# Performance work log

Measured on AMD Instinct MI355X. Metric: run time of the kernel, lower is better.

## Reference

```python
import jax, jax.numpy as jnp
import numpy as np

HEADS = 8
EPS = 1e-5

def setup_inputs() -> dict:
    key = jax.random.key(0)
    ks = jax.random.split(key, 4)
    B, S, N, C = 1, 256, 384, 512
    msa = jax.random.normal(ks[0], (B, S, N, C), dtype=jnp.float32)
    mask = jnp.ones((B, S), dtype=jnp.int32)
    Wqkv = jax.random.normal(ks[1], (3 * C, C), dtype=jnp.float32) * (C ** -0.5)
    bqkv = jnp.zeros((3 * C,), dtype=jnp.float32)
    Wout = jax.random.normal(ks[2], (C, C), dtype=jnp.float32) * (C ** -0.5)
    bout = jnp.zeros((C,), dtype=jnp.float32)
    gamma = jnp.ones((C,), dtype=jnp.float32)
    beta = jnp.zeros((C,), dtype=jnp.float32)
    return {"msa": msa, "mask": mask, "Wqkv": Wqkv, "bqkv": bqkv,
            "Wout": Wout, "bout": bout, "gamma": gamma, "beta": beta}

def reference(msa, mask, Wqkv, bqkv, Wout, bout, gamma, beta):
    B, S, N, C = msa.shape
    H = HEADS
    Dh = C // H
    scale = Dh ** -0.5
    msa_t = jnp.transpose(msa, (0, 2, 1, 3))            # [B,N,S,C]
    qkv = msa_t @ Wqkv.T + bqkv                          # [B,N,S,3C]
    qkv = qkv.reshape(B, N, S, 3, H, Dh)
    q, k, v = qkv[..., 0, :, :], qkv[..., 1, :, :], qkv[..., 2, :, :]  # [B,N,S,H,Dh]
    attn = jnp.einsum('bnshc,bnthc->bhst', q, k) * scale  # reduce over N and head-dim
    attn = jnp.where(mask[:, None, None, :] == 0, -1e9, attn)
    attn = jax.nn.softmax(attn, axis=-1)                 # [B,H,S,S]
    out = jnp.einsum('bhst,bnthc->bnshc', attn, v).reshape(B, N, S, C)
    out = jnp.transpose(out, (0, 2, 1, 3))               # [B,S,N,C]
    out = out @ Wout.T + bout
    x = msa + out
    mu = jnp.mean(x, axis=-1, keepdims=True)
    var = jnp.mean((x - mu) ** 2, axis=-1, keepdims=True)
    return (x - mu) * jax.lax.rsqrt(var + EPS) * gamma + beta
```

## Files before the change

kernel.cpp:

```cpp
#include <hip/hip_runtime.h>

#define S_ 256
#define N_ 384
#define C_ 512
#define H_ 8
#define R_ (N_*S_)
#define SPLITK 16
#define NPK (N_/SPLITK)

typedef _Float16 f16;
typedef _Float16 f16x8 __attribute__((ext_vector_type(8)));
typedef _Float16 f16x4 __attribute__((ext_vector_type(4)));
typedef float f32x4 __attribute__((ext_vector_type(4)));

#define MFMA16(a,b,c) __builtin_amdgcn_mfma_f32_16x16x32_f16(a,b,c,0,0,0)

typedef __attribute__((address_space(3))) unsigned int as3_u32;
typedef __attribute__((address_space(1))) const unsigned int as1_u32;

__device__ __forceinline__ void gl_lds16(const void* g, void* l) {
    __builtin_amdgcn_global_load_lds((as1_u32*)(unsigned long long)g,
                                     (as3_u32*)(unsigned long long)l, 16, 0, 0);
}

__device__ __forceinline__ int swz_off(int row, int g) {
    return row*64 + (((g) ^ (row & 7)) << 3);
}

__global__ __launch_bounds__(256) void k_prep(const float* __restrict__ Wqkv,
                                              const float* __restrict__ Wout,
                                              f16* __restrict__ Wq16, f16* __restrict__ Wo16) {
    int i = blockIdx.x * 256 + threadIdx.x;
    if (i < 1536 * C_) Wq16[i] = (f16)Wqkv[i];
    if (i < C_ * C_)   Wo16[i] = (f16)Wout[i];
}

__global__ __launch_bounds__(256) void k_cast(const float* __restrict__ msa,
                                              f16* __restrict__ msaT) {
    int t = blockIdx.x * 256 + threadIdx.x;
    int r = t >> 6, cg = t & 63;
    int n = r >> 8, s = r & 255;
    const float* src = msa + (s * N_ + n) * C_ + (cg << 3);
    float4 lo = *(const float4*)src;
    float4 hi = *(const float4*)(src + 4);
    f16x8 v;
    v[0]=(f16)lo.x; v[1]=(f16)lo.y; v[2]=(f16)lo.z; v[3]=(f16)lo.w;
    v[4]=(f16)hi.x; v[5]=(f16)hi.y; v[6]=(f16)hi.z; v[7]=(f16)hi.w;
    *(f16x8*)(msaT + r * C_ + (cg << 3)) = v;
}

__global__ __launch_bounds__(256) void k_qkv(const f16* __restrict__ msaT,
                                             const f16* __restrict__ W,
                                             const float* __restrict__ bqkv,
                                             f16* __restrict__ qk,
                                             f16* __restrict__ vT) {
    int wg = (blockIdx.x & 7) * 1152 + (blockIdx.x >> 3);
    int bx = wg / 12, by = wg % 12;
    int j0 = by << 7;
    int tid = threadIdx.x, lane = tid & 63, wid = tid >> 6;
    int wr = (wid >> 1) << 6, wc = (wid & 1) << 6;
    __shared__ f16 As[128 * 64];
    __shared__ f16 Bs[128 * 64];
    const f16* Abase = msaT + (bx << 7) * C_;
    const f16* Bbase = W + j0 * C_;
    f32x4 acc[4][4] = {};
    for (int kt = 0; kt < 8; ++kt) {
        int c0 = kt << 6;
        __syncthreads();
#pragma unroll
        for (int i = 0; i < 4; ++i) {
            int id = (i << 8) + tid;
            int row = id >> 3, g = (id & 7) ^ (row & 7);
            int lofs = ((i << 8) + (wid << 6)) << 4;
            gl_lds16(Abase + row * C_ + c0 + (g << 3), (char*)As + lofs);
            gl_lds16(Bbase + row * C_ + c0 + (g << 3), (char*)Bs + lofs);
        }
        __syncthreads();
#pragma unroll
        for (int ks = 0; ks < 64; ks += 32) {
            int kg = (ks >> 3) + (lane >> 4);
            f16x8 af[4], bf[4];
#pragma unroll
            for (int m = 0; m < 4; ++m)
                af[m] = *(const f16x8*)&As[swz_off(wr + (m << 4) + (lane & 15), kg)];
#pragma unroll
            for (int j = 0; j < 4; ++j)
                bf[j] = *(const f16x8*)&Bs[swz_off(wc + (j << 4) + (lane & 15), kg)];
#pragma unroll
            for (int m = 0; m < 4; ++m)
#pragma unroll
                for (int j = 0; j < 4; ++j)
                    acc[m][j] = MFMA16(af[m], bf[j], acc[m][j]);
        }
    }
#pragma unroll
    for (int m = 0; m < 4; ++m) {
        int rloc = wr + (m << 4) + ((lane >> 4) << 2);
        int r0 = (bx << 7) + rloc;
        if (by < 8) {
#pragma unroll
            for (int j = 0; j < 4; ++j) {
                int jc = j0 + wc + (j << 4) + (lane & 15);
                float bv = bqkv[jc];
#pragma unroll
                for (int q = 0; q < 4; ++q)
                    qk[(r0 + q) * 1024 + jc] = (f16)(acc[m][j][q] + bv);
            }
        } else {
            int n = bx >> 1, sBase = ((bx & 1) << 7) + rloc;
#pragma unroll
            for (int j = 0; j < 4; ++j) {
                int jl = (j0 - 1024) + wc + (j << 4) + (lane & 15);
                float bv = bqkv[1024 + jl];
                f16x4 vv;
#pragma unroll
                for (int q = 0; q < 4; ++q) vv[q] = (f16)(acc[m][j][q] + bv);
                *(f16x4*)(vT + ((n * H_ + (jl >> 6)) * 64 + (jl & 63)) * S_ + sBase) = vv;
            }
        }
    }
}

__global__ __launch_bounds__(256) void k_logits(const f16* __restrict__ qk,
                                                float* __restrict__ logP) {
    int wg = (blockIdx.x & 7) * 64 + (blockIdx.x >> 3);
    int sk = wg >> 5, rem = wg & 31, h = rem >> 2, sb = (rem >> 1) & 1, tb = rem & 1;
    int s0 = sb << 7, t0 = tb << 7, n0 = sk * NPK;
    int tid = threadIdx.x, lane = tid & 63, wid = tid >> 6;
    int wr = (wid >> 1) << 6, wc = (wid & 1) << 6;
    __shared__ f16 As[128 * 64];
    __shared__ f16 Bs[128 * 64];
    f32x4 acc[4][4] = {};
    for (int ni = 0; ni < NPK; ++ni) {
        int n = n0 + ni;
        const f16* Abase = qk + (n * S_ + s0) * 1024 + (h << 6);
        const f16* Bbase = qk + (n * S_ + t0) * 1024 + 512 + (h << 6);
        __syncthreads();
#pragma unroll
        for (int i = 0; i < 4; ++i) {
            int id = (i << 8) + tid;
            int row = id >> 3, g = (id & 7) ^ (row & 7);
            int lofs = ((i << 8) + (wid << 6)) << 4;
            gl_lds16(Abase + row * 1024 + (g << 3), (char*)As + lofs);
            gl_lds16(Bbase + row * 1024 + (g << 3), (char*)Bs + lofs);
        }
        __syncthreads();
#pragma unroll
        for (int ks = 0; ks < 64; ks += 32) {
            int kg = (ks >> 3) + (lane >> 4);
            f16x8 af[4], bf[4];
#pragma unroll
            for (int m = 0; m < 4; ++m)
                af[m] = *(const f16x8*)&As[swz_off(wr + (m << 4) + (lane & 15), kg)];
#pragma unroll
            for (int j = 0; j < 4; ++j)
                bf[j] = *(const f16x8*)&Bs[swz_off(wc + (j << 4) + (lane & 15), kg)];
#pragma unroll
            for (int m = 0; m < 4; ++m)
#pragma unroll
                for (int j = 0; j < 4; ++j)
                    acc[m][j] = MFMA16(af[m], bf[j], acc[m][j]);
        }
    }
#pragma unroll
    for (int m = 0; m < 4; ++m) {
        int rloc = wr + (m << 4) + ((lane >> 4) << 2);
#pragma unroll
        for (int j = 0; j < 4; ++j) {
            int tc = t0 + wc + (j << 4) + (lane & 15);
#pragma unroll
            for (int q = 0; q < 4; ++q)
                logP[((sk * H_ + h) * S_ + s0 + rloc + q) * S_ + tc] = acc[m][j][q];
        }
    }
}

__global__ __launch_bounds__(256) void k_softmax(const float* __restrict__ logP,
                                                 const int* __restrict__ mask,
                                                 f16* __restrict__ attn) {
    int hs = blockIdx.x;
    int t = threadIdx.x, lane = t & 63, wid = t >> 6;
    float v = 0.f;
#pragma unroll
    for (int sk = 0; sk < SPLITK; ++sk)
        v += logP[(sk * H_ * S_ + hs) * S_ + t];
    v *= 0.125f;
    if (mask[t] == 0) v = -1e9f;
    __shared__ float redm[4], reds[4];
    float m_ = v;
    for (int o = 32; o > 0; o >>= 1) m_ = fmaxf(m_, __shfl_xor(m_, o));
    if (lane == 0) redm[wid] = m_;
    __syncthreads();
    float bm = fmaxf(fmaxf(redm[0], redm[1]), fmaxf(redm[2], redm[3]));
    float e = __expf(v - bm);
    float s_ = e;
    for (int o = 32; o > 0; o >>= 1) s_ += __shfl_xor(s_, o);
    if (lane == 0) reds[wid] = s_;
    __syncthreads();
    float tot = reds[0] + reds[1] + reds[2] + reds[3];
    attn[hs * S_ + t] = (f16)(e / tot);
}

__global__ __launch_bounds__(256) void k_pv(const f16* __restrict__ attn,
                                            const f16* __restrict__ vT,
                                            f16* __restrict__ attn_out) {
    int n = blockIdx.x >> 3, h = blockIdx.x & 7;
    int tid = threadIdx.x, lane = tid & 63, wid = tid >> 6;
    __shared__ f16 As[256 * 32];
    __shared__ f16 Bs[64 * 32];
    f32x4 acc[4][4] = {};
    for (int tt = 0; tt < 8; ++tt) {
        int t0 = tt << 5;
        __syncthreads();
#pragma unroll
        for (int i = 0; i < 4; ++i) {
            int id = tid + (i << 8);
            int sr = id >> 2, c4 = id & 3;
            *(f16x8*)&As[sr * 32 + (c4 << 3)] =
                *(const f16x8*)(attn + (h * S_ + sr) * S_ + t0 + (c4 << 3));
        }
        {
            int d = tid >> 2, c4 = tid & 3;
            *(f16x8*)&Bs[d * 32 + (c4 << 3)] =
                *(const f16x8*)(vT + ((n * H_ + h) * 64 + d) * S_ + t0 + (c4 << 3));
        }
        __syncthreads();
        f16x8 af[4], bf[4];
#pragma unroll
        for (int m = 0; m < 4; ++m)
            af[m] = *(const f16x8*)&As[(wid * 64 + m * 16 + (lane & 15)) * 32 + ((lane >> 4) << 3)];
#pragma unroll
        for (int j = 0; j < 4; ++j)
            bf[j] = *(const f16x8*)&Bs[(j * 16 + (lane & 15)) * 32 + ((lane >> 4) << 3)];
#pragma unroll
        for (int m = 0; m < 4; ++m)
#pragma unroll
            for (int j = 0; j < 4; ++j)
                acc[m][j] = MFMA16(af[m], bf[j], acc[m][j]);
    }
#pragma unroll
    for (int m = 0; m < 4; ++m) {
        int sl = wid * 64 + m * 16 + ((lane >> 4) << 2);
#pragma unroll
        for (int j = 0; j < 4; ++j) {
            int d = j * 16 + (lane & 15);
#pragma unroll
            for (int q = 0; q < 4; ++q)
                attn_out[(n * S_ + sl + q) * C_ + h * 64 + d] = (f16)acc[m][j][q];
        }
    }
}

__global__ __launch_bounds__(512) void k_out_ln(const f16* __restrict__ attn_out,
                                                const f16* __restrict__ Wo,
                                                const float* __restrict__ bout,
                                                const f16* __restrict__ msaT,
                                                const float* __restrict__ gamma,
                                                const float* __restrict__ beta,
                                                float* __restrict__ out) {
    int r0 = blockIdx.x << 6;
    int n = r0 >> 8, s0 = r0 & 255;
    int tid = threadIdx.x, lane = tid & 63, wid = tid >> 6;
    __shared__ f16 As[64 * 32];
    __shared__ f16 Bs[512 * 32];
    __shared__ float redS[8][64], redQ[8][64], muS[64], rsS[64];
    f32x4 acc[4][4] = {};
    for (int kt = 0; kt < 16; ++kt) {
        int c0 = kt << 5;
        __syncthreads();
        if (tid < 256) {
            int row = tid >> 2, c4 = tid & 3;
            *(f16x8*)&As[row * 32 + (c4 << 3)] =
                *(const f16x8*)(attn_out + (r0 + row) * C_ + c0 + (c4 << 3));
        }
#pragma unroll
        for (int i = 0; i < 4; ++i) {
            int id = tid + (i << 9);
            int row = id >> 2, c4 = id & 3;
            *(f16x8*)&Bs[row * 32 + (c4 << 3)] =
                *(const f16x8*)(Wo + row * C_ + c0 + (c4 << 3));
        }
        __syncthreads();
        f16x8 af[4], bf[4];
#pragma unroll
        for (int m = 0; m < 4; ++m)
            af[m] = *(const f16x8*)&As[((m << 4) + (lane & 15)) * 32 + ((lane >> 4) << 3)];
#pragma unroll
        for (int j = 0; j < 4; ++j)
            bf[j] = *(const f16x8*)&Bs[((wid << 6) + (j << 4) + (lane & 15)) * 32 + ((lane >> 4) << 3)];
#pragma unroll
        for (int m = 0; m < 4; ++m)
#pragma unroll
            for (int j = 0; j < 4; ++j)
                acc[m][j] = MFMA16(af[m], bf[j], acc[m][j]);
    }
    float psum[4][4] = {}, psq[4][4] = {};
#pragma unroll
    for (int m = 0; m < 4; ++m)
#pragma unroll
        for (int j = 0; j < 4; ++j) {
            int c = (wid << 6) + (j << 4) + (lane & 15);
            float bj = bout[c];
#pragma unroll
            for (int q = 0; q < 4; ++q) {
                int rl = (m << 4) + ((lane >> 4) << 2) + q;
                float x = acc[m][j][q] + bj + (float)msaT[(r0 + rl) * C_ + c];
                acc[m][j][q] = x;
                psum[m][q] += x;
                psq[m][q] += x * x;
            }
        }
#pragma unroll
    for (int m = 0; m < 4; ++m)
#pragma unroll
        for (int q = 0; q < 4; ++q)
            for (int o = 1; o < 16; o <<= 1) {
                psum[m][q] += __shfl_xor(psum[m][q], o);
                psq[m][q]  += __shfl_xor(psq[m][q], o);
            }
    if ((lane & 15) == 0) {
#pragma unroll
        for (int m = 0; m < 4; ++m)
#pragma unroll
            for (int q = 0; q < 4; ++q) {
                int rl = (m << 4) + ((lane >> 4) << 2) + q;
                redS[wid][rl] = psum[m][q];
                redQ[wid][rl] = psq[m][q];
            }
    }
    __syncthreads();
    if (tid < 64) {
        float t1 = 0.f, t2 = 0.f;
#pragma unroll
        for (int w = 0; w < 8; ++w) { t1 += redS[w][tid]; t2 += redQ[w][tid]; }
        float mu = t1 * (1.0f / 512.0f);
        float var = t2 * (1.0f / 512.0f) - mu * mu;
        muS[tid] = mu;
        rsS[tid] = rsqrtf(var + 1e-5f);
    }
    __syncthreads();
#pragma unroll
    for (int m = 0; m < 4; ++m)
#pragma unroll
        for (int j = 0; j < 4; ++j) {
            int c = (wid << 6) + (j << 4) + (lane & 15);
            float g = gamma[c], bb = beta[c];
#pragma unroll
            for (int q = 0; q < 4; ++q) {
                int rl = (m << 4) + ((lane >> 4) << 2) + q;
                int s = s0 + rl;
                float y = (acc[m][j][q] - muS[rl]) * rsS[rl] * g + bb;
                out[(s * N_ + n) * C_ + c] = y;
            }
        }
}

extern "C" void kernel_launch(void* const* d_in, const int* in_sizes, int n_in,
                              void* d_out, int out_size, void* d_ws, size_t ws_size,
                              hipStream_t stream) {
    const float* msa   = (const float*)d_in[0];
    const int*   mask  = (const int*)d_in[1];
    const float* Wqkv  = (const float*)d_in[2];
    const float* bqkv  = (const float*)d_in[3];
    const float* Wout  = (const float*)d_in[4];
    const float* bout  = (const float*)d_in[5];
    const float* gamma = (const float*)d_in[6];
    const float* beta  = (const float*)d_in[7];
    float* out = (float*)d_out;
    char* ws = (char*)d_ws;

    f16*   qk   = (f16*)(ws);
    f16*   vT   = (f16*)(ws + 201326592);
    f16*   msaT = (f16*)(ws + 301989888);
    float* logP = (float*)(ws + 402653184);
    f16*   attn = (f16*)(ws + 436207616);
    f16*   Wq16 = (f16*)(ws + 437256192);
    f16*   Wo16 = (f16*)(ws + 438829056);
    f16*   attn_out = qk;

    k_prep<<<dim3(3072), dim3(256), 0, stream>>>(Wqkv, Wout, Wq16, Wo16);
    k_cast<<<dim3(24576), dim3(256), 0, stream>>>(msa, msaT);
    k_qkv<<<dim3(9216), dim3(256), 0, stream>>>(msaT, Wq16, bqkv, qk, vT);
    k_logits<<<dim3(512), dim3(256), 0, stream>>>(qk, logP);
    k_softmax<<<dim3(2048), dim3(256), 0, stream>>>(logP, mask, attn);
    k_pv<<<dim3(3072), dim3(256), 0, stream>>>(attn, vT, attn_out);
    k_out_ln<<<dim3(1536), dim3(512), 0, stream>>>(attn_out, Wo16, bout, msaT, gamma, beta, out);
}
```

Baseline: 667.5 us.

## Double-buffer LDS tiles with K=32 stages in QKV and logits GEMMs

Splits each 64-wide K tile into two 32-wide stages and double-buffers them in LDS, so the async global-to-LDS loads for the next stage are issued before the MFMA work on the current stage. One of the two barriers per iteration goes away, and the new layout uses a swizzle adapted to 32-element rows. Each stage now carries half the MFMA work, so there are twice as many barriers in total, and the smaller XOR swizzle may change the LDS bank-conflict pattern.

```diff
diff --git a/kernel.cpp b/kernel.cpp
--- a/kernel.cpp
+++ b/kernel.cpp
@@ -23,8 +23,40 @@
                                      (as3_u32*)(unsigned long long)l, 16, 0, 0);
 }
 
-__device__ __forceinline__ int swz_off(int row, int g) {
-    return row*64 + (((g) ^ (row & 7)) << 3);
+__device__ __forceinline__ void stage_tile(const f16* __restrict__ Ab,
+                                           const f16* __restrict__ Bb,
+                                           int stride, f16* As_, f16* Bs_,
+                                           int tid, int wid) {
+#pragma unroll
+    for (int i = 0; i < 2; ++i) {
+        int id = (i << 8) + tid;
+        int row = id >> 2;
+        int g = (id & 3) ^ ((row >> 1) & 3);
+        int lofs = ((i << 8) + (wid << 6)) << 4;
+        gl_lds16(Ab + row * stride + (g << 3), (char*)As_ + lofs);
+        gl_lds16(Bb + row * stride + (g << 3), (char*)Bs_ + lofs);
+    }
+}
+
+__device__ __forceinline__ void frag_mma(const f16* As_, const f16* Bs_,
+                                         int lane, int wr, int wc, f32x4 acc[4][4]) {
+    int kg = lane >> 4;
+    f16x8 af[4], bf[4];
+#pragma unroll
+    for (int m = 0; m < 4; ++m) {
+        int row = wr + (m << 4) + (lane & 15);
+        af[m] = *(const f16x8*)&As_[row * 32 + ((kg ^ ((row >> 1) & 3)) << 3)];
+    }
+#pragma unroll
+    for (int j = 0; j < 4; ++j) {
+        int row = wc + (j << 4) + (lane & 15);
+        bf[j] = *(const f16x8*)&Bs_[row * 32 + ((kg ^ ((row >> 1) & 3)) << 3)];
+    }
+#pragma unroll
+    for (int m = 0; m < 4; ++m)
+#pragma unroll
+        for (int j = 0; j < 4; ++j)
+            acc[m][j] = MFMA16(af[m], bf[j], acc[m][j]);
 }
 
 __global__ __launch_bounds__(256) void k_prep(const float* __restrict__ Wqkv,
@@ -59,39 +91,20 @@
     int j0 = by << 7;
     int tid = threadIdx.x, lane = tid & 63, wid = tid >> 6;
     int wr = (wid >> 1) << 6, wc = (wid & 1) << 6;
-    __shared__ f16 As[128 * 64];
-    __shared__ f16 Bs[128 * 64];
+    __shared__ f16 As[2][128 * 32];
+    __shared__ f16 Bs[2][128 * 32];
     const f16* Abase = msaT + (bx << 7) * C_;
     const f16* Bbase = W + j0 * C_;
     f32x4 acc[4][4] = {};
-    for (int kt = 0; kt < 8; ++kt) {
-        int c0 = kt << 6;
-        __syncthreads();
-#pragma unroll
-        for (int i = 0; i < 4; ++i) {
-            int id = (i << 8) + tid;
-            int row = id >> 3, g = (id & 7) ^ (row & 7);
-            int lofs = ((i << 8) + (wid << 6)) << 4;
-            gl_lds16(Abase + row * C_ + c0 + (g << 3), (char*)As + lofs);
-            gl_lds16(Bbase + row * C_ + c0 + (g << 3), (char*)Bs + lofs);
-        }
-        __syncthreads();
-#pragma unroll
-        for (int ks = 0; ks < 64; ks += 32) {
-            int kg = (ks >> 3) + (lane >> 4);
-            f16x8 af[4], bf[4];
-#pragma unroll
-            for (int m = 0; m < 4; ++m)
-                af[m] = *(const f16x8*)&As[swz_off(wr + (m << 4) + (lane & 15), kg)];
-#pragma unroll
-            for (int j = 0; j < 4; ++j)
-                bf[j] = *(const f16x8*)&Bs[swz_off(wc + (j << 4) + (lane & 15), kg)];
-#pragma unroll
-            for (int m = 0; m < 4; ++m)
-#pragma unroll
-                for (int j = 0; j < 4; ++j)
-                    acc[m][j] = MFMA16(af[m], bf[j], acc[m][j]);
-        }
+    stage_tile(Abase, Bbase, C_, As[0], Bs[0], tid, wid);
+    __syncthreads();
+    for (int t = 0; t < 16; ++t) {
+        int cur = t & 1;
+        if (t < 15)
+            stage_tile(Abase + ((t + 1) << 5), Bbase + ((t + 1) << 5), C_,
+                       As[cur ^ 1], Bs[cur ^ 1], tid, wid);
+        frag_mma(As[cur], Bs[cur], lane, wr, wc, acc);
+        __syncthreads();
     }
 #pragma unroll
     for (int m = 0; m < 4; ++m) {
@@ -128,39 +141,24 @@
     int s0 = sb << 7, t0 = tb << 7, n0 = sk * NPK;
     int tid = threadIdx.x, lane = tid & 63, wid = tid >> 6;
     int wr = (wid >> 1) << 6, wc = (wid & 1) << 6;
-    __shared__ f16 As[128 * 64];
-    __shared__ f16 Bs[128 * 64];
+    __shared__ f16 As[2][128 * 32];
+    __shared__ f16 Bs[2][128 * 32];
+    const f16* Aroot = qk + s0 * 1024 + (h << 6);
+    const f16* Broot = qk + t0 * 1024 + 512 + (h << 6);
     f32x4 acc[4][4] = {};
-    for (int ni = 0; ni < NPK; ++ni) {
-        int n = n0 + ni;
-        const f16* Abase = qk + (n * S_ + s0) * 1024 + (h << 6);
-        const f16* Bbase = qk + (n * S_ + t0) * 1024 + 512 + (h << 6);
-        __syncthreads();
-#pragma unroll
-        for (int i = 0; i < 4; ++i) {
-            int id = (i << 8) + tid;
-            int row = id >> 3, g = (id & 7) ^ (row & 7);
-            int lofs = ((i << 8) + (wid << 6)) << 4;
-            gl_lds16(Abase + row * 1024 + (g << 3), (char*)As + lofs);
-            gl_lds16(Bbase + row * 1024 + (g << 3), (char*)Bs + lofs);
-        }
-        __syncthreads();
-#pragma unroll
-        for (int ks = 0; ks < 64; ks += 32) {
-            int kg = (ks >> 3) + (lane >> 4);
-            f16x8 af[4], bf[4];
-#pragma unroll
-            for (int m = 0; m < 4; ++m)
-                af[m] = *(const f16x8*)&As[swz_off(wr + (m << 4) + (lane & 15), kg)];
-#pragma unroll
-            for (int j = 0; j < 4; ++j)
-                bf[j] = *(const f16x8*)&Bs[swz_off(wc + (j << 4) + (lane & 15), kg)];
-#pragma unroll
-            for (int m = 0; m < 4; ++m)
-#pragma unroll
-                for (int j = 0; j < 4; ++j)
-                    acc[m][j] = MFMA16(af[m], bf[j], acc[m][j]);
-        }
+    stage_tile(Aroot + n0 * S_ * 1024, Broot + n0 * S_ * 1024, 1024,
+               As[0], Bs[0], tid, wid);
+    __syncthreads();
+    for (int t = 0; t < 2 * NPK; ++t) {
+        int cur = t & 1;
+        if (t < 2 * NPK - 1) {
+            int tn = t + 1;
+            int n = n0 + (tn >> 1), dh = (tn & 1) << 5;
+            stage_tile(Aroot + n * S_ * 1024 + dh, Broot + n * S_ * 1024 + dh, 1024,
+                       As[cur ^ 1], Bs[cur ^ 1], tid, wid);
+        }
+        frag_mma(As[cur], Bs[cur], lane, wr, wc, acc);
+        __syncthreads();
     }
 #pragma unroll
     for (int m = 0; m < 4; ++m) {
```

Result: faster. 635.7 us (-4.8%).
